# Kernel optimization log

Measured on AMD Instinct MI355X. Metric: run time of the kernel, lower is better.

Reference implementation:

```python
import jax, jax.numpy as jnp
import numpy as np
import math

N_FFT = 1024
HOP = 256
N_FRAMES = 16384
SR = 24000
FFT_BIN = N_FFT // 2 + 1
EPS = 1e-11


def hann(n):
    # torch.hann_window default (periodic=True)
    return 0.5 * (1.0 - jnp.cos(2.0 * jnp.pi * jnp.arange(n, dtype=jnp.float32) / n))


def linear_interp(x, scale):
    # x: [B, T] -> [B, T*scale]; matches F.interpolate(mode='linear', align_corners=False)
    T = x.shape[-1]
    pos = (jnp.arange(T * scale, dtype=jnp.float32) + 0.5) / scale - 0.5
    pos = jnp.clip(pos, 0.0, T - 1.0)
    lo = jnp.floor(pos).astype(jnp.int32)
    hi = jnp.minimum(lo + 1, T - 1)
    frac = pos - lo.astype(jnp.float32)
    return x[:, lo] * (1.0 - frac) + x[:, hi] * frac


def impulse_train(f0, hop_length, sample_rate):
    # f0: [B, n_frames] -> impulse train [B, n_frames*hop]
    f0_up = linear_interp(f0, hop_length)
    phase = jnp.cumsum(f0_up, axis=-1) / sample_rate
    saw = jnp.mod(phase, 1.0)
    imp = saw - jnp.roll(saw, -1, axis=-1) + f0_up / sample_rate
    # original runs under torch.no_grad()
    return jax.lax.stop_gradient(imp)


def stft(x, n_fft, hop, window):
    # torch.stft(center=True, pad_mode='reflect', onesided, normalized=False)
    pad = n_fft // 2
    xp = jnp.pad(x, ((0, 0), (pad, pad)), mode="reflect")
    nf = (xp.shape[-1] - n_fft) // hop + 1
    idx = jnp.arange(nf)[:, None] * hop + jnp.arange(n_fft)[None, :]
    frames = xp[:, idx] * window  # [B, nf, n_fft]
    return jnp.fft.rfft(frames, axis=-1).transpose(0, 2, 1)  # [B, bins, nf]


def istft(S, n_fft, hop, window):
    # torch.istft(center=True): windowed overlap-add, divide by sum of squared windows
    B = S.shape[0]
    frames = jnp.fft.irfft(S.transpose(0, 2, 1), n=n_fft, axis=-1) * window  # [B, nf, n_fft]
    nf = frames.shape[1]
    out_len = n_fft + (nf - 1) * hop
    idx = jnp.arange(nf)[:, None] * hop + jnp.arange(n_fft)[None, :]
    sig = jnp.zeros((B, out_len), frames.dtype).at[:, idx].add(frames)
    wsq = jnp.zeros((out_len,), frames.dtype).at[idx].add(
        jnp.broadcast_to(window * window, (nf, n_fft))
    )
    pad = n_fft // 2
    return sig[:, pad:-pad] / jnp.maximum(wsq[pad:-pad], EPS)


def spectral_envelope_filter(signal, envelope, n_fft, hop):
    w = hann(n_fft)
    S = stft(signal, n_fft, hop, w)[:, :, 1:]  # drop first frame -> [B, bins, n_frames]
    return istft(S * envelope, n_fft, hop, w)


def estimate_minimum_phase(amp):
    # amp: [B, bins, T] real positive envelope; cepstral min-phase along dim 1
    n = (amp.shape[1] - 1) * 2
    cep = jnp.fft.irfft(jnp.log(amp), n=n, axis=1)
    fold = jnp.concatenate(
        [jnp.ones((1,), jnp.float32),
         2.0 * jnp.ones((n // 2 - 1,), jnp.float32),
         jnp.ones((1,), jnp.float32),
         jnp.zeros((n // 2 - 1,), jnp.float32)]
    )
    cep = cep * fold[None, :, None]
    return jnp.exp(jnp.fft.rfft(cep, axis=1))  # complex min-phase spectrum [B, bins, T]


def setup_inputs() -> dict:
    key = jax.random.key(0)
    k1, k2, k3 = jax.random.split(key, 3)
    log_f0 = jnp.full((1, N_FRAMES), math.log(100.0), dtype=jnp.float32)
    spec_env_noi = jax.random.normal(k1, (1, FFT_BIN, N_FRAMES), jnp.float32) - 6.0
    spec_env_per = jax.random.normal(k2, (1, FFT_BIN, N_FRAMES), jnp.float32) - 6.0
    noise = jax.random.normal(k3, (1, HOP * N_FRAMES), jnp.float32)
    return {"log_f0": log_f0, "spec_env_noi": spec_env_noi,
            "spec_env_per": spec_env_per, "noise": noise}


def reference(log_f0, spec_env_noi, spec_env_per, noise):
    pulse = impulse_train(jnp.exp(log_f0), HOP, SR)
    noi = spectral_envelope_filter(noise, jnp.exp(spec_env_noi), N_FFT, HOP)
    per = spectral_envelope_filter(
        pulse, estimate_minimum_phase(jnp.exp(spec_env_per)), N_FFT, HOP
    )
    return noi + per  # [1, (N_FRAMES-1)*HOP]
```

## Files before the change

kernel.cpp:

```cpp
#include <hip/hip_runtime.h>
#include <math.h>

#define L_TOT 4194304
#define NFR   16384
#define OUTN  4194048


__device__ __forceinline__ int lvl_off(int a) {
  return L_TOT - (L_TOT >> (a - 1));
}

__device__ __forceinline__ int swz(int e) {
  int h = (e >> 4) & 3, g = (e >> 6) & 3, f = (e >> 8) & 3;
  return e ^ (h * 5) ^ (g * 3) ^ ((f * 12) & 15);
}

__device__ __forceinline__ int dr4(int p) {
  return ((p & 3) << 8) | (((p >> 2) & 3) << 6) | (((p >> 4) & 3) << 4) |
         (((p >> 6) & 3) << 2) | ((p >> 8) & 3);
}

__device__ __forceinline__ float f0_up_val(const float* f0arr, int j) {
  float pos = __fadd_rn(__fmul_rn(__fadd_rn((float)j, 0.5f), 1.0f / 256.0f), -0.5f);
  pos = fminf(fmaxf(pos, 0.0f), 16383.0f);
  int lo = (int)pos;
  int hi = min(lo + 1, NFR - 1);
  float frac = __fadd_rn(pos, -(float)lo);
  float a = __fmul_rn(f0arr[lo], __fadd_rn(1.0f, -frac));
  float b = __fmul_rn(f0arr[hi], frac);
  return __fadd_rn(a, b);
}

__device__ __forceinline__ float f0_up_local(const float* Fl, int w0, int j) {
  float pos = __fadd_rn(__fmul_rn(__fadd_rn((float)j, 0.5f), 1.0f / 256.0f), -0.5f);
  pos = fminf(fmaxf(pos, 0.0f), 16383.0f);
  int lo = (int)pos;
  int hi = min(lo + 1, NFR - 1);
  float frac = __fadd_rn(pos, -(float)lo);
  float a = __fmul_rn(Fl[lo - w0], __fadd_rn(1.0f, -frac));
  float b = __fmul_rn(Fl[hi - w0], frac);
  return __fadd_rn(a, b);
}

__global__ __launch_bounds__(256) void tree_kernel(const float* __restrict__ logf0,
                                                   float* __restrict__ W,
                                                   float* __restrict__ out) {
  int tid = threadIdx.x;
  int bid = blockIdx.x;
  if (bid < 2) {
    int g = bid * 256 + tid;
    double a = (double)g * 3.14159265358979323846 / 512.0;
    W[2 * L_TOT + g] = (float)cos(a);
    W[2 * L_TOT + 512 + g] = (float)sin(a);
  }
  if (bid >= 2 && bid < 66) {
    int g = (bid - 2) * 256 + tid;
    W[2 * L_TOT + 2048 + g] = (float)exp((double)logf0[g]);
  }
  {
    int base_o = bid * 2048;
#pragma unroll
    for (int k = 0; k < 2; ++k) {
      int off = base_o + k * 1024 + tid * 4;
      if (off < OUTN) *(float4*)&out[off] = make_float4(0.f, 0.f, 0.f, 0.f);
    }
  }
  __shared__ float Fl[10];
  __shared__ float A[2048];
  __shared__ float B[1024];
  int base = bid * 2048;
  int w0 = (base >> 8) - 1;
  if (tid < 10) {
    int f = min(max(w0 + tid, 0), NFR - 1);
    Fl[tid] = (float)exp((double)logf0[f]);
  }
  __syncthreads();
  for (int i = tid; i < 2048; i += 256) A[i] = f0_up_local(Fl, w0, base + i);
  __syncthreads();
  float* src = A;
  float* dst = B;
  int cnt = 1024;
  for (int a = 1; a <= 11; ++a) {
    int gbase = base >> a;
    for (int i = tid; i < cnt; i += 256) {
      float v = __fadd_rn(src[2 * i], src[2 * i + 1]);
      dst[i] = v;
      if (a == 11) W[lvl_off(11) + gbase + i] = v;
    }
    __syncthreads();
    float* tmp = src; src = dst; dst = tmp;
    cnt >>= 1;
  }
}

__device__ __forceinline__ float prefix_top(const float* TT, const float* f0arr, int m) {
  float acc = 0.0f;
  bool first = true;
  int pos = 0;
  for (int a = 22; a >= 12; --a) {
    if (m & (1 << a)) {
      float node = TT[2048 - (4096 >> (a - 11)) + (pos >> a)];
      acc = first ? node : __fadd_rn(acc, node);
      first = false;
      pos += (1 << a);
    }
  }
  if (m & 1) {
    float node = f0_up_val(f0arr, pos);
    acc = first ? node : __fadd_rn(acc, node);
  }
  return acc;
}

__global__ __launch_bounds__(256) void pulse_kernel(float* W) {
  const float* f0arr = W + 2 * L_TOT + 2048;
  __shared__ float TT[2047];
  __shared__ float Tl[510];
  __shared__ float P[4100];
  int tid = threadIdx.x;
  int base = blockIdx.x * 4096;

  for (int i = tid; i < 2048; i += 256) P[i] = W[lvl_off(11) + i];
  __syncthreads();
  for (int i = tid; i < 1024; i += 256) TT[i] = __fadd_rn(P[2 * i], P[2 * i + 1]);
  __syncthreads();
  {
    int off_prev = 0, cnt = 512;
    for (int a = 13; a <= 22; ++a) {
      int off = 2048 - (4096 >> (a - 11));
      for (int i = tid; i < cnt; i += 256)
        TT[off + i] = __fadd_rn(TT[off_prev + 2 * i], TT[off_prev + 2 * i + 1]);
      __syncthreads();
      off_prev = off;
      cnt >>= 1;
    }
  }

  float v[16];
#pragma unroll
  for (int c = 0; c < 16; ++c) v[c] = f0_up_val(f0arr, base + 16 * tid + c);
  float s2[8], s4[4], s8[2];
#pragma unroll
  for (int j = 0; j < 8; ++j) s2[j] = __fadd_rn(v[2 * j], v[2 * j + 1]);
#pragma unroll
  for (int j = 0; j < 4; ++j) s4[j] = __fadd_rn(s2[2 * j], s2[2 * j + 1]);
  s8[0] = __fadd_rn(s4[0], s4[1]);
  s8[1] = __fadd_rn(s4[2], s4[3]);
  Tl[tid] = __fadd_rn(s8[0], s8[1]);
  __syncthreads();
  if (tid < 128) Tl[256 + tid] = __fadd_rn(Tl[2 * tid], Tl[2 * tid + 1]);
  __syncthreads();
  if (tid < 64)  Tl[384 + tid] = __fadd_rn(Tl[256 + 2 * tid], Tl[256 + 2 * tid + 1]);
  __syncthreads();
  if (tid < 32)  Tl[448 + tid] = __fadd_rn(Tl[384 + 2 * tid], Tl[384 + 2 * tid + 1]);
  __syncthreads();
  if (tid < 16)  Tl[480 + tid] = __fadd_rn(Tl[448 + 2 * tid], Tl[448 + 2 * tid + 1]);
  __syncthreads();
  if (tid < 8)   Tl[496 + tid] = __fadd_rn(Tl[480 + 2 * tid], Tl[480 + 2 * tid + 1]);
  __syncthreads();
  if (tid < 4)   Tl[504 + tid] = __fadd_rn(Tl[496 + 2 * tid], Tl[496 + 2 * tid + 1]);
  __syncthreads();
  if (tid < 2)   Tl[508 + tid] = __fadd_rn(Tl[504 + 2 * tid], Tl[504 + 2 * tid + 1]);
  __syncthreads();

  float accT = 0.0f;
  bool firstT = true;
  {
    int pos = 0;
    for (int a = 22; a >= 12; --a) {
      if (base & (1 << a)) {
        float node = TT[2048 - (4096 >> (a - 11)) + (pos >> a)];
        accT = firstT ? node : __fadd_rn(accT, node);
        firstT = false;
        pos += (1 << a);
      }
    }
  }
  float accM = accT;
  bool firstM = firstT;
  {
    int rh = 16 * tid;
    int lpos = 0;
    for (int a = 11; a >= 4; --a) {
      if (rh & (1 << a)) {
        float node = Tl[512 - (512 >> (a - 4)) + (lpos >> a)];
        accM = firstM ? node : __fadd_rn(accM, node);
        firstM = false;
        lpos += (1 << a);
      }
    }
  }
  if (tid >= 1) P[16 * tid] = accM;
#pragma unroll
  for (int c = 1; c <= 15; ++c) {
    float acc = accM;
    bool first = firstM;
    int lp = 0;
    if (c & 8) { float n = s8[lp >> 3]; acc = first ? n : __fadd_rn(acc, n); first = false; lp += 8; }
    if (c & 4) { float n = s4[lp >> 2]; acc = first ? n : __fadd_rn(acc, n); first = false; lp += 4; }
    if (c & 2) { float n = s2[lp >> 1]; acc = first ? n : __fadd_rn(acc, n); first = false; lp += 2; }
    if (c & 1) { float n = v[lp];       acc = first ? n : __fadd_rn(acc, n); }
    P[16 * tid + c] = acc;
  }
  if (tid == 0) P[4096] = prefix_top(TT, f0arr, base + 4096);
  if (tid == 1) {
    int m2 = base + 4097;
    P[4097] = (m2 <= L_TOT) ? prefix_top(TT, f0arr, m2) : 0.0f;
  }
  __syncthreads();

  float o[16];
#pragma unroll
  for (int c = 0; c < 16; ++c) {
    int i = base + 16 * tid + c;
    float P1 = P[16 * tid + c + 1];
    float P2 = (i == L_TOT - 1) ? f0_up_val(f0arr, 0)
                                : P[16 * tid + c + 2];
    float t1 = __fdiv_rn(P1, 24000.0f);
    float saw1 = __fadd_rn(t1, -floorf(t1));
    float t2 = __fdiv_rn(P2, 24000.0f);
    float saw2 = __fadd_rn(t2, -floorf(t2));
    float cc = __fdiv_rn(v[c], 24000.0f);
    o[c] = __fadd_rn(__fadd_rn(saw1, -saw2), cc);
  }
#pragma unroll
  for (int k = 0; k < 4; ++k)
    *(float4*)&W[L_TOT + base + 16 * tid + 4 * k] =
        make_float4(o[4 * k], o[4 * k + 1], o[4 * k + 2], o[4 * k + 3]);
}

template <int DIR>
__device__ __forceinline__ void bfly_dif(float2* F, int e0, int e1, int e2, int e3,
                                         float ur, float ui) {
  if (DIR < 0) ui = -ui;
  float2 x0 = F[e0], x1 = F[e1], x2 = F[e2], x3 = F[e3];
  float s0r = x0.x + x2.x, s0i = x0.y + x2.y;
  float s1r = x1.x + x3.x, s1i = x1.y + x3.y;
  float d0r = x0.x - x2.x, d0i = x0.y - x2.y;
  float ddr = x1.x - x3.x, ddi = x1.y - x3.y;
  float t3r = (DIR > 0) ? -ddi : ddi;
  float t3i = (DIR > 0) ? ddr : -ddr;
  float vr = ur * ur - ui * ui, vi = 2.0f * ur * ui;
  float w3r = ur * vr - ui * vi, w3i = ur * vi + ui * vr;
  F[e0] = make_float2(s0r + s1r, s0i + s1i);
  float a1r = d0r + t3r, a1i = d0i + t3i;
  F[e1] = make_float2(a1r * ur - a1i * ui, a1r * ui + a1i * ur);
  float a2r = s0r - s1r, a2i = s0i - s1i;
  F[e2] = make_float2(a2r * vr - a2i * vi, a2r * vi + a2i * vr);
  float a3r = d0r - t3r, a3i = d0i - t3i;
  F[e3] = make_float2(a3r * w3r - a3i * w3i, a3r * w3i + a3i * w3r);
  __syncthreads();
}

template <int DIR>
__device__ __forceinline__ void bfly_dit(float2* F, int e0, int e1, int e2, int e3,
                                         float ur, float ui) {
  if (DIR < 0) ui = -ui;
  float2 x0 = F[e0], x1 = F[e1], x2 = F[e2], x3 = F[e3];
  float vr = ur * ur - ui * ui, vi = 2.0f * ur * ui;
  float w3r = ur * vr - ui * vi, w3i = ur * vi + ui * vr;
  float b1r = x1.x * ur - x1.y * ui, b1i = x1.x * ui + x1.y * ur;
  float b2r = x2.x * vr - x2.y * vi, b2i = x2.x * vi + x2.y * vr;
  float b3r = x3.x * w3r - x3.y * w3i, b3i = x3.x * w3i + x3.y * w3r;
  float s0r = x0.x + b2r, s0i = x0.y + b2i;
  float d0r = x0.x - b2r, d0i = x0.y - b2i;
  float s1r = b1r + b3r, s1i = b1i + b3i;
  float ddr = b1r - b3r, ddi = b1i - b3i;
  float d1r = (DIR > 0) ? -ddi : ddi;
  float d1i = (DIR > 0) ? ddr : -ddr;
  F[e0] = make_float2(s0r + s1r, s0i + s1i);
  F[e1] = make_float2(d0r + d1r, d0i + d1i);
  F[e2] = make_float2(s0r - s1r, s0i - s1i);
  F[e3] = make_float2(d0r - d1r, d0i - d1i);
  __syncthreads();
}

__device__ __forceinline__ float hann_w(int i, const float2* T0) {
  int j = (i > 512) ? (1024 - i) : i;
  float c = (j <= 256) ? T0[j].x : -T0[512 - j].x;
  return 0.5f - 0.5f * c;
}

__device__ __forceinline__ float edge_scale(int t, const float2* T0) {
  int p = t + 512;
  int jmin = max(0, (p - 768) >> 8);
  int jmax = min(NFR - 1, p >> 8);
  float wsq = 0.0f;
  for (int j = jmin; j <= jmax; ++j) {
    float w = hann_w(p - 256 * j, T0);
    wsq += w * w;
  }
  return 1.5f / fmaxf(wsq, 1e-11f);
}

__device__ __forceinline__ void combine_one(int k, float An, const float2* F, float2* H) {
  int k2 = (1024 - k) & 1023;
  float2 z = F[swz(dr4(k))], mm = F[swz(dr4(k2))];
  float Ar = 0.5f * (z.x + mm.x), Ai = 0.5f * (z.y - mm.y);
  float Br = 0.5f * (z.y + mm.y), Bi = 0.5f * (mm.x - z.x);
  float2 h = H[k];
  H[k] = make_float2(Br * h.x - Bi * h.y + Ar * An,
                     Br * h.y + Bi * h.x + Ai * An);
}

__global__ __launch_bounds__(256) void column_kernel(
    const float* __restrict__ noise,
    const float* __restrict__ envn,
    const float* __restrict__ envp,
    const float* __restrict__ W,
    float* __restrict__ out) {
  __shared__ float2 F[1024];
  __shared__ float2 hA[513], hB[513];
  __shared__ float2 TW[341];
  int tid = threadIdx.x;
  int bid = blockIdx.x;
  int g = (bid & 7) * 1024 + (bid >> 3);
  int fA = 2 * g;
  const float* pulse = W + L_TOT;
  const float* gtab = W + 2 * L_TOT;
  const float2* T0 = TW;
  const float2* T1 = TW + 257;
  const float2* T2 = TW + 321;
  const float2* T3 = TW + 337;

  for (int i = tid; i < 341; i += 256) {
    int e;
    if (i < 257) e = i;
    else if (i < 321) e = (i - 257) << 2;
    else if (i < 337) e = (i - 321) << 4;
    else e = (i - 337) << 6;
    TW[i] = make_float2(gtab[e], gtab[512 + e]);
  }
  for (int k = tid; k < 513; k += 256) {
    float2 e = *(const float2*)&envp[k * NFR + fA];
    hA[k] = e;
  }

  int a00 = swz(tid), a01 = swz(tid + 256), a02 = swz(tid + 512), a03 = swz(tid + 768);
  int b1_ = ((tid >> 6) << 8) | (tid & 63);
  int a10 = swz(b1_), a11 = swz(b1_ + 64), a12 = swz(b1_ + 128), a13 = swz(b1_ + 192);
  int b2_ = ((tid >> 4) << 6) | (tid & 15);
  int a20 = swz(b2_), a21 = swz(b2_ + 16), a22 = swz(b2_ + 32), a23 = swz(b2_ + 48);
  int b3_ = ((tid >> 2) << 4) | (tid & 3);
  int a30 = swz(b3_), a31 = swz(b3_ + 4), a32 = swz(b3_ + 8), a33 = swz(b3_ + 12);
  int q_ = tid << 2;
  int a40 = swz(q_), a41 = swz(q_ + 1), a42 = swz(q_ + 2), a43 = swz(q_ + 3);
  __syncthreads();

  F[a00] = hA[tid];
  F[a01] = hA[tid + 256];
  F[a02] = (tid == 0) ? hA[512] : hA[512 - tid];
  F[a03] = hA[256 - tid];
  __syncthreads();
  { float2 t_ = T0[tid];      bfly_dif<+1>(F, a00, a01, a02, a03, t_.x, t_.y); }
  { float2 t_ = T1[tid & 63]; bfly_dif<+1>(F, a10, a11, a12, a13, t_.x, t_.y); }
  { float2 t_ = T2[tid & 15]; bfly_dif<+1>(F, a20, a21, a22, a23, t_.x, t_.y); }
  { float2 t_ = T3[tid & 3];  bfly_dif<+1>(F, a30, a31, a32, a33, t_.x, t_.y); }
  {
    int drt = ((tid & 3) << 6) | (((tid >> 2) & 3) << 4) |
              (((tid >> 4) & 3) << 2) | ((tid >> 6) & 3);
    float2 x0 = F[a40], x1 = F[a41], x2 = F[a42], x3 = F[a43];
    float s0r = x0.x + x2.x, s0i = x0.y + x2.y;
    float s1r = x1.x + x3.x, s1i = x1.y + x3.y;
    float d0r = x0.x - x2.x, d0i = x0.y - x2.y;
    float ddr = x1.x - x3.x, ddi = x1.y - x3.y;
    float y0r = s0r + s1r, y0i = s0i + s1i;
    float y1r = d0r - ddi, y1i = d0i + ddr;
    float y2r = s0r - s1r, y2i = s0i - s1i;
    float sc0 = (drt == 0) ? (1.0f / 1024.0f) : (2.0f / 1024.0f);
    float sc2 = (drt == 0) ? (1.0f / 1024.0f) : 0.0f;
    y0r *= sc0; y0i *= sc0;
    y1r *= (2.0f / 1024.0f); y1i *= (2.0f / 1024.0f);
    y2r *= sc2; y2i *= sc2;
    float S0r = y0r + y2r, S0i = y0i + y2i;
    float D0r = y0r - y2r, D0i = y0i - y2i;
    float D1r = y1i, D1i = -y1r;
    F[a40] = make_float2(S0r + y1r, S0i + y1i);
    F[a41] = make_float2(D0r + D1r, D0i + D1i);
    F[a42] = make_float2(S0r - y1r, S0i - y1i);
    F[a43] = make_float2(D0r - D1r, D0i - D1i);
  }
  __syncthreads();
  { float2 t_ = T3[tid & 3];  bfly_dit<-1>(F, a30, a31, a32, a33, t_.x, t_.y); }
  { float2 t_ = T2[tid & 15]; bfly_dit<-1>(F, a20, a21, a22, a23, t_.x, t_.y); }
  { float2 t_ = T1[tid & 63]; bfly_dit<-1>(F, a10, a11, a12, a13, t_.x, t_.y); }
  { float2 t_ = T0[tid];      bfly_dit<-1>(F, a00, a01, a02, a03, t_.x, t_.y); }
  {
    int k2 = (1024 - tid) & 1023;
    float2 z = F[a00], mm = F[swz(k2)];
    float GAr = 0.5f * (z.x + mm.x), GAi = 0.5f * (z.y - mm.y);
    float GBr = 0.5f * (z.y + mm.y), GBi = 0.5f * (mm.x - z.x);
    float er = expf(GAr);
    float si, co;
    sincosf(GAi, &si, &co);
    hA[tid] = make_float2(er * co, er * si);
    er = expf(GBr);
    sincosf(GBi, &si, &co);
    hB[tid] = make_float2(er * co, er * si);

    z = F[a01]; mm = F[swz(768 - tid)];
    GAr = 0.5f * (z.x + mm.x); GAi = 0.5f * (z.y - mm.y);
    GBr = 0.5f * (z.y + mm.y); GBi = 0.5f * (mm.x - z.x);
    er = expf(GAr);
    sincosf(GAi, &si, &co);
    hA[tid + 256] = make_float2(er * co, er * si);
    er = expf(GBr);
    sincosf(GBi, &si, &co);
    hB[tid + 256] = make_float2(er * co, er * si);

    if (tid == 0) {
      z = F[a02];
      GAr = 0.5f * (z.x + z.x); GAi = 0.0f;
      GBr = 0.5f * (z.y + z.y); GBi = 0.0f;
      er = expf(GAr);
      sincosf(GAi, &si, &co);
      hA[512] = make_float2(er * co, er * si);
      er = expf(GBr);
      sincosf(GBi, &si, &co);
      hB[512] = make_float2(er * co, er * si);
    }
  }
  __syncthreads();

#define PACK_FRAME(QOFF, J, ADDR)                                      \
  {                                                                    \
    int i = tid + 256 * (J);                                           \
    int q = (QOFF) + i;                                                \
    if (q < 0) q = -q;                                                 \
    else if (q >= L_TOT) q = 2 * L_TOT - 2 - q;                        \
    float wv = hann_w(i, T0);                                          \
    F[ADDR] = make_float2(noise[q] * wv, pulse[q] * wv);               \
  }
  PACK_FRAME(256 * fA - 256, 0, a00)
  PACK_FRAME(256 * fA - 256, 1, a01)
  PACK_FRAME(256 * fA - 256, 2, a02)
  PACK_FRAME(256 * fA - 256, 3, a03)
  __syncthreads();
  { float2 t_ = T0[tid];      bfly_dif<-1>(F, a00, a01, a02, a03, t_.x, t_.y); }
  { float2 t_ = T1[tid & 63]; bfly_dif<-1>(F, a10, a11, a12, a13, t_.x, t_.y); }
  { float2 t_ = T2[tid & 15]; bfly_dif<-1>(F, a20, a21, a22, a23, t_.x, t_.y); }
  { float2 t_ = T3[tid & 3];  bfly_dif<-1>(F, a30, a31, a32, a33, t_.x, t_.y); }
  bfly_dif<-1>(F, a40, a41, a42, a43, 1.0f, 0.0f);
  float2 eA0 = *(const float2*)&envn[tid * NFR + fA];
  combine_one(tid, expf(eA0.x), F, hA);
  float2 eA1 = *(const float2*)&envn[(tid + 256) * NFR + fA];
  combine_one(tid + 256, expf(eA1.x), F, hA);
  float2 eA2 = make_float2(0.0f, 0.0f);
  if (tid == 0) {
    eA2 = *(const float2*)&envn[512 * NFR + fA];
    combine_one(512, expf(eA2.x), F, hA);
  }
  __syncthreads();

  PACK_FRAME(256 * fA, 0, a00)
  PACK_FRAME(256 * fA, 1, a01)
  PACK_FRAME(256 * fA, 2, a02)
  PACK_FRAME(256 * fA, 3, a03)
  __syncthreads();
  { float2 t_ = T0[tid];      bfly_dif<-1>(F, a00, a01, a02, a03, t_.x, t_.y); }
  { float2 t_ = T1[tid & 63]; bfly_dif<-1>(F, a10, a11, a12, a13, t_.x, t_.y); }
  { float2 t_ = T2[tid & 15]; bfly_dif<-1>(F, a20, a21, a22, a23, t_.x, t_.y); }
  { float2 t_ = T3[tid & 3];  bfly_dif<-1>(F, a30, a31, a32, a33, t_.x, t_.y); }
  bfly_dif<-1>(F, a40, a41, a42, a43, 1.0f, 0.0f);
  combine_one(tid, expf(eA0.y), F, hB);
  combine_one(tid + 256, expf(eA1.y), F, hB);
  if (tid == 0) combine_one(512, expf(eA2.y), F, hB);
  __syncthreads();

#pragma unroll
  for (int j = 0; j < 4; ++j) {
    int i = tid + 256 * j;
    float2 zv;
    if (i <= 512) {
      zv = make_float2(hA[i].x - hB[i].y, hA[i].y + hB[i].x);
    } else {
      int jj = 1024 - i;
      zv = make_float2(hA[jj].x + hB[jj].y, hB[jj].x - hA[jj].y);
    }
    F[swz(dr4(i))] = zv;
  }
  __syncthreads();
  bfly_dit<+1>(F, a40, a41, a42, a43, 1.0f, 0.0f);
  { float2 t_ = T3[tid & 3];  bfly_dit<+1>(F, a30, a31, a32, a33, t_.x, t_.y); }
  { float2 t_ = T2[tid & 15]; bfly_dit<+1>(F, a20, a21, a22, a23, t_.x, t_.y); }
  { float2 t_ = T1[tid & 63]; bfly_dit<+1>(F, a10, a11, a12, a13, t_.x, t_.y); }
  { float2 t_ = T0[tid];      bfly_dit<+1>(F, a00, a01, a02, a03, t_.x, t_.y); }
  const float scl = 1.0f / 1536.0f;
  {
    float2 f0v = F[a00], f1v = F[a01], f2v = F[a02], f3v = F[a03];
    float hw0 = hann_w(tid, T0) * scl;
    float hw1 = hann_w(tid + 256, T0) * scl;
    float hw2 = hann_w(tid + 512, T0) * scl;
    float hw3 = hann_w(tid + 768, T0) * scl;
    int tb = 256 * fA - 512 + tid;
    float val;
    int t;
    t = tb;
    val = f0v.x * hw0;
    if (t >= 0) {
      if (t < 256) val *= edge_scale(t, T0);
      atomicAdd(&out[t], val);
    }
    t = tb + 256;
    val = f1v.x * hw1 + f0v.y * hw0;
    if (t >= 0 && t < OUTN) {
      if (t < 256 || t >= OUTN - 256) val *= edge_scale(t, T0);
      atomicAdd(&out[t], val);
    }
    t = tb + 512;
    val = f2v.x * hw2 + f1v.y * hw1;
    if (t < OUTN) {
      if (t < 256 || t >= OUTN - 256) val *= edge_scale(t, T0);
      atomicAdd(&out[t], val);
    }
    t = tb + 768;
    val = f3v.x * hw3 + f2v.y * hw2;
    if (t < OUTN) {
      if (t >= OUTN - 256) val *= edge_scale(t, T0);
      atomicAdd(&out[t], val);
    }
    t = tb + 1024;
    val = f3v.y * hw3;
    if (t < OUTN) {
      if (t >= OUTN - 256) val *= edge_scale(t, T0);
      atomicAdd(&out[t], val);
    }
  }
#undef PACK_FRAME
}

extern "C" void kernel_launch(void* const* d_in, const int* in_sizes, int n_in,
                              void* d_out, int out_size, void* d_ws, size_t ws_size,
                              hipStream_t stream) {
  const float* logf0 = (const float*)d_in[0];
  const float* envn  = (const float*)d_in[1];
  const float* envp  = (const float*)d_in[2];
  const float* noise = (const float*)d_in[3];
  float* out = (float*)d_out;
  float* W = (float*)d_ws;

  tree_kernel<<<dim3(2048), dim3(256), 0, stream>>>(logf0, W, out);
  pulse_kernel<<<dim3(L_TOT / 4096), dim3(256), 0, stream>>>(W);
  column_kernel<<<dim3(NFR / 2), dim3(256), 0, stream>>>(noise, envn, envp, W, out);
}
```

Baseline: 225.6 us.

## Replace block barriers with wave fences in wave-local FFT stages

The block-wide __syncthreads is taken out of every radix-4 butterfly. Stages whose data exchange stays inside one 64-thread wave (the inner stages) now use only a wave barrier, and full block barriers remain only where data crosses waves. This cuts workgroup synchronisation stalls across the many FFT passes per frame. The impulse-train epilogue also computes each sawtooth value once instead of twice per sample. The change relies on wave-lockstep LDS visibility, which is subtle to get right.

```diff
diff --git a/kernel.cpp b/kernel.cpp
--- a/kernel.cpp
+++ b/kernel.cpp
@@ -4,6 +4,8 @@
 #define L_TOT 4194304
 #define NFR   16384
 #define OUTN  4194048
+
+#define WAVE_FENCE() __builtin_amdgcn_wave_barrier()
 
 
 __device__ __forceinline__ int lvl_off(int a) {
@@ -209,19 +211,24 @@
   }
   __syncthreads();
 
+  float sw[17];
+#pragma unroll
+  for (int k = 1; k <= 17; ++k) {
+    float Pv;
+    if (k <= 16) {
+      Pv = P[16 * tid + k];
+    } else {
+      Pv = (base + 16 * tid + 17 > L_TOT) ? f0_up_val(f0arr, 0)
+                                          : P[16 * tid + 17];
+    }
+    float t1 = __fdiv_rn(Pv, 24000.0f);
+    sw[k - 1] = __fadd_rn(t1, -floorf(t1));
+  }
   float o[16];
 #pragma unroll
   for (int c = 0; c < 16; ++c) {
-    int i = base + 16 * tid + c;
-    float P1 = P[16 * tid + c + 1];
-    float P2 = (i == L_TOT - 1) ? f0_up_val(f0arr, 0)
-                                : P[16 * tid + c + 2];
-    float t1 = __fdiv_rn(P1, 24000.0f);
-    float saw1 = __fadd_rn(t1, -floorf(t1));
-    float t2 = __fdiv_rn(P2, 24000.0f);
-    float saw2 = __fadd_rn(t2, -floorf(t2));
     float cc = __fdiv_rn(v[c], 24000.0f);
-    o[c] = __fadd_rn(__fadd_rn(saw1, -saw2), cc);
+    o[c] = __fadd_rn(__fadd_rn(sw[c], -sw[c + 1]), cc);
   }
 #pragma unroll
   for (int k = 0; k < 4; ++k)
@@ -249,7 +256,6 @@
   F[e2] = make_float2(a2r * vr - a2i * vi, a2r * vi + a2i * vr);
   float a3r = d0r - t3r, a3i = d0i - t3i;
   F[e3] = make_float2(a3r * w3r - a3i * w3i, a3r * w3i + a3i * w3r);
-  __syncthreads();
 }
 
 template <int DIR>
@@ -272,7 +278,6 @@
   F[e1] = make_float2(d0r + d1r, d0i + d1i);
   F[e2] = make_float2(s0r - s1r, s0i - s1i);
   F[e3] = make_float2(d0r - d1r, d0i - d1i);
-  __syncthreads();
 }
 
 __device__ __forceinline__ float hann_w(int i, const float2* T0) {
@@ -351,11 +356,14 @@
   F[a01] = hA[tid + 256];
   F[a02] = (tid == 0) ? hA[512] : hA[512 - tid];
   F[a03] = hA[256 - tid];
-  __syncthreads();
   { float2 t_ = T0[tid];      bfly_dif<+1>(F, a00, a01, a02, a03, t_.x, t_.y); }
+  __syncthreads();
   { float2 t_ = T1[tid & 63]; bfly_dif<+1>(F, a10, a11, a12, a13, t_.x, t_.y); }
+  WAVE_FENCE();
   { float2 t_ = T2[tid & 15]; bfly_dif<+1>(F, a20, a21, a22, a23, t_.x, t_.y); }
+  WAVE_FENCE();
   { float2 t_ = T3[tid & 3];  bfly_dif<+1>(F, a30, a31, a32, a33, t_.x, t_.y); }
+  WAVE_FENCE();
   {
     int drt = ((tid & 3) << 6) | (((tid >> 2) & 3) << 4) |
               (((tid >> 4) & 3) << 2) | ((tid >> 6) & 3);
@@ -380,11 +388,15 @@
     F[a42] = make_float2(S0r - y1r, S0i - y1i);
     F[a43] = make_float2(D0r - D1r, D0i - D1i);
   }
-  __syncthreads();
+  WAVE_FENCE();
   { float2 t_ = T3[tid & 3];  bfly_dit<-1>(F, a30, a31, a32, a33, t_.x, t_.y); }
+  WAVE_FENCE();
   { float2 t_ = T2[tid & 15]; bfly_dit<-1>(F, a20, a21, a22, a23, t_.x, t_.y); }
+  WAVE_FENCE();
   { float2 t_ = T1[tid & 63]; bfly_dit<-1>(F, a10, a11, a12, a13, t_.x, t_.y); }
+  __syncthreads();
   { float2 t_ = T0[tid];      bfly_dit<-1>(F, a00, a01, a02, a03, t_.x, t_.y); }
+  __syncthreads();
   {
     int k2 = (1024 - tid) & 1023;
     float2 z = F[a00], mm = F[swz(k2)];
@@ -435,12 +447,16 @@
   PACK_FRAME(256 * fA - 256, 1, a01)
   PACK_FRAME(256 * fA - 256, 2, a02)
   PACK_FRAME(256 * fA - 256, 3, a03)
-  __syncthreads();
   { float2 t_ = T0[tid];      bfly_dif<-1>(F, a00, a01, a02, a03, t_.x, t_.y); }
+  __syncthreads();
   { float2 t_ = T1[tid & 63]; bfly_dif<-1>(F, a10, a11, a12, a13, t_.x, t_.y); }
+  WAVE_FENCE();
   { float2 t_ = T2[tid & 15]; bfly_dif<-1>(F, a20, a21, a22, a23, t_.x, t_.y); }
+  WAVE_FENCE();
   { float2 t_ = T3[tid & 3];  bfly_dif<-1>(F, a30, a31, a32, a33, t_.x, t_.y); }
+  WAVE_FENCE();
   bfly_dif<-1>(F, a40, a41, a42, a43, 1.0f, 0.0f);
+  __syncthreads();
   float2 eA0 = *(const float2*)&envn[tid * NFR + fA];
   combine_one(tid, expf(eA0.x), F, hA);
   float2 eA1 = *(const float2*)&envn[(tid + 256) * NFR + fA];
@@ -456,12 +472,16 @@
   PACK_FRAME(256 * fA, 1, a01)
   PACK_FRAME(256 * fA, 2, a02)
   PACK_FRAME(256 * fA, 3, a03)
-  __syncthreads();
   { float2 t_ = T0[tid];      bfly_dif<-1>(F, a00, a01, a02, a03, t_.x, t_.y); }
+  __syncthreads();
   { float2 t_ = T1[tid & 63]; bfly_dif<-1>(F, a10, a11, a12, a13, t_.x, t_.y); }
+  WAVE_FENCE();
   { float2 t_ = T2[tid & 15]; bfly_dif<-1>(F, a20, a21, a22, a23, t_.x, t_.y); }
+  WAVE_FENCE();
   { float2 t_ = T3[tid & 3];  bfly_dif<-1>(F, a30, a31, a32, a33, t_.x, t_.y); }
+  WAVE_FENCE();
   bfly_dif<-1>(F, a40, a41, a42, a43, 1.0f, 0.0f);
+  __syncthreads();
   combine_one(tid, expf(eA0.y), F, hB);
   combine_one(tid + 256, expf(eA1.y), F, hB);
   if (tid == 0) combine_one(512, expf(eA2.y), F, hB);
@@ -481,9 +501,13 @@
   }
   __syncthreads();
   bfly_dit<+1>(F, a40, a41, a42, a43, 1.0f, 0.0f);
+  WAVE_FENCE();
   { float2 t_ = T3[tid & 3];  bfly_dit<+1>(F, a30, a31, a32, a33, t_.x, t_.y); }
+  WAVE_FENCE();
   { float2 t_ = T2[tid & 15]; bfly_dit<+1>(F, a20, a21, a22, a23, t_.x, t_.y); }
+  WAVE_FENCE();
   { float2 t_ = T1[tid & 63]; bfly_dit<+1>(F, a10, a11, a12, a13, t_.x, t_.y); }
+  __syncthreads();
   { float2 t_ = T0[tid];      bfly_dit<+1>(F, a00, a01, a02, a03, t_.x, t_.y); }
   const float scl = 1.0f / 1536.0f;
   {
```

Result: slower. 230.2 us (+2.0%).
